# Performance work log

Hardware: AMD Instinct MI355X
Metric: run time of the kernel (lower is better)

The kernel has to match this reference:

```python
import jax, jax.numpy as jnp
import numpy as np

P = 16          # patch_size
EMBED = 768     # embed_dim
HEAD_DIM = 64   # embed_dim // num_heads
ROPE_BASE = 10000.0


def rope_2d(coords, head_dim, base):
    """Axial 2D RoPE. coords: (N, 2) int -> cos, sin each (N, head_dim).
    head_dim is split evenly over the two axes; within an axis, frequency
    pairs are repeated twice (standard rotate-pairs layout)."""
    dpa = head_dim // 2                                   # dims per axis
    inv_freq = 1.0 / (base ** (jnp.arange(0, dpa, 2, dtype=jnp.float32) / dpa))  # (dpa//2,)
    ang = coords.astype(jnp.float32)[:, :, None] * inv_freq[None, None, :]       # (N, 2, dpa//2)
    ang = jnp.repeat(ang, 2, axis=-1).reshape(coords.shape[0], head_dim)          # (N, head_dim)
    return jnp.cos(ang), jnp.sin(ang)


def setup_inputs() -> dict:
    key = jax.random.key(0)
    k1, k2 = jax.random.split(key, 2)
    B, C, H, W = 32, 3, 512, 512
    images = jax.random.normal(k1, (B, C, H, W), dtype=jnp.float32)
    patch_dim = C * P * P
    W_proj = jax.random.normal(k2, (patch_dim, EMBED), dtype=jnp.float32) * (patch_dim ** -0.5)
    b_proj = jnp.zeros((EMBED,), dtype=jnp.float32)
    return {"images": images, "W_proj": W_proj, "b_proj": b_proj}


def reference(images, W_proj, b_proj):
    B, C, H, W = images.shape
    Hp, Wp = H // P, W // P
    N = B * Hp * Wp
    # patchify: c (hp p1) (wp p2) -> (hp wp) (c p1 p2), packed across batch
    x = images.reshape(B, C, Hp, P, Wp, P).transpose(0, 2, 4, 1, 3, 5).reshape(N, C * P * P)
    tokens = x @ W_proj + b_proj                              # (N, EMBED)
    # per-image patch coordinates (identical grid for every image)
    ys, xs = jnp.meshgrid(jnp.arange(Hp), jnp.arange(Wp), indexing='ij')
    coords = jnp.stack([ys, xs], axis=-1).reshape(Hp * Wp, 2)
    patch_coords = jnp.tile(coords, (B, 1))                    # (N, 2)
    rope_cos, rope_sin = rope_2d(patch_coords, HEAD_DIM, ROPE_BASE)
    cu_seqlens = (jnp.arange(B + 1, dtype=jnp.int32) * (Hp * Wp))
    is_patch = jnp.ones((N,), dtype=bool)
    return tokens, cu_seqlens, patch_coords, rope_cos, rope_sin, is_patch
```

## Files before the change

### kernel.cpp

```cpp
#include <hip/hip_runtime.h>
#include <hip/hip_bf16.h>

typedef unsigned short u16;
typedef unsigned int   u32;
typedef __bf16 bf16x8 __attribute__((ext_vector_type(8)));
typedef float  f32x4  __attribute__((ext_vector_type(4)));

#define N_TOK 32768
constexpr long long OFF_TOKENS = 0;
constexpr long long OFF_CU     = 25165824LL;
constexpr long long OFF_COORDS = 25165857LL;
constexpr long long OFF_COS    = 25231393LL;
constexpr long long OFF_SIN    = 27328545LL;
constexpr long long OFF_ISP    = 29425697LL;

__device__ __forceinline__ void split_bf16(float v, u16& h, u16& l) {
    __hip_bfloat16 bh = __float2bfloat16(v);
    float fh = __bfloat162float(bh);
    __hip_bfloat16 bl = __float2bfloat16(v - fh);
    h = __builtin_bit_cast(u16, bh);
    l = __builtin_bit_cast(u16, bl);
}

__device__ __forceinline__ u32 pk2(float lo, float hi) {
    u32 a = (u32)__builtin_bit_cast(u16, __float2bfloat16(lo));
    u32 b = (u32)__builtin_bit_cast(u16, __float2bfloat16(hi));
    return a | (b << 16);
}

__global__ __launch_bounds__(256) void prep_w(const float* __restrict__ W,
                                              u16* __restrict__ wt2) {
    const int bid = blockIdx.x;
    const int bn  = bid / 24;
    const int kt  = bid - bn * 24;
    const int t   = threadIdx.x;
    #pragma unroll
    for (int p = 0; p < 2; p++) {
        const int idx  = t + p * 256;
        const int lane = idx & 63;
        const int j    = (idx >> 6) & 1;
        const int wnq  = idx >> 7;
        const int n    = bn * 128 + wnq * 32 + j * 16 + (lane & 15);
        const int k0   = kt * 32 + (lane >> 4) * 8;
        u16 hv[8], lv[8];
        #pragma unroll
        for (int e = 0; e < 8; e++)
            split_bf16(W[(size_t)(k0 + e) * 768 + n], hv[e], lv[e]);
        uint4 H, L;
        H.x = (u32)hv[0] | ((u32)hv[1] << 16); H.y = (u32)hv[2] | ((u32)hv[3] << 16);
        H.z = (u32)hv[4] | ((u32)hv[5] << 16); H.w = (u32)hv[6] | ((u32)hv[7] << 16);
        L.x = (u32)lv[0] | ((u32)lv[1] << 16); L.y = (u32)lv[2] | ((u32)lv[3] << 16);
        L.z = (u32)lv[4] | ((u32)lv[5] << 16); L.w = (u32)lv[6] | ((u32)lv[7] << 16);
        u16* dst = wt2 + (size_t)bid * 8192 + (((wnq << 12) | (j << 10) | (lane << 4)) >> 1);
        *(uint4*)dst          = H;
        *(uint4*)(dst + 1024) = L;
    }
}

__global__ __launch_bounds__(512, 4) void patch_gemm_mfma(
    const float* __restrict__ img, const u16* __restrict__ wt2,
    const float* __restrict__ bias, float* __restrict__ out)
{
    __shared__ __align__(16) char smem[16384];
    char* pA0 = smem;
    char* pA1 = smem + 8192;

    const int L   = blockIdx.x;
    const int c   = (L & 7) * 192 + (L >> 3);
    const int bm  = c / 6;
    const int bn  = c - bm * 6;
    const int tb  = bn * 24;

    const int tid  = threadIdx.x;
    const int lane = tid & 63;
    const int wid  = tid >> 6;
    const int wm   = (wid >> 2) << 6;
    const int wn   = (wid & 3) << 5;
    const int lr   = lane & 15;
    const int lg   = lane >> 4;

    const int am = tid & 127;
    const int aq = tid >> 7;
    const int m  = bm * 128 + am;
    const int bb = m >> 10;
    const int hp = (m & 1023) >> 5;
    const int wq = m & 31;
    const float* abase = img + (size_t)bb * 786432 + (size_t)hp * 8192 + wq * 16;
    const int a_wb = am * 64 + (((aq >> 1) ^ ((am >> 3) & 1)) << 5) + ((aq & 1) << 4);

    const int a_rd = lr * 64 + (((lg >> 1) ^ ((lr >> 3) & 1)) << 5) + ((lg & 1) << 4);

    const char* bfrag = (const char*)wt2 + ((wid & 3) << 12) + (lane << 4);

    f32x4 acc[4][2];
    #pragma unroll
    for (int i = 0; i < 4; i++)
        #pragma unroll
        for (int j = 0; j < 2; j++) acc[i][j] = {0.f, 0.f, 0.f, 0.f};

    float4 A0a, A0b, A1a, A1b;

#define LOAD_A(ra, rb, T)                                                   \
    {   const float* ap = abase + ((T) >> 3) * 262144 +                     \
            (((T) & 7) * 2 + (aq >> 1)) * 512 + (aq & 1) * 8;               \
        ra = *(const float4*)ap;  rb = *(const float4*)(ap + 4); }

#define CVT_STORE(ra, rb, pdst)                                             \
    {   uint4 Hq;                                                           \
        Hq.x = pk2(ra.x, ra.y); Hq.y = pk2(ra.z, ra.w);                     \
        Hq.z = pk2(rb.x, rb.y); Hq.w = pk2(rb.z, rb.w);                     \
        *(uint4*)((pdst) + a_wb) = Hq; }

#define ITER(T, Ca, Cb, La, Lb, PACV, PAC)                                  \
    {   bf16x8 bhf[2], blf[2];                                              \
        {   const char* s = bfrag + (size_t)(tb + (T)) * 16384;             \
            bhf[0] = *(const bf16x8*)(s);                                   \
            bhf[1] = *(const bf16x8*)(s + 1024);                            \
            blf[0] = *(const bf16x8*)(s + 2048);                            \
            blf[1] = *(const bf16x8*)(s + 3072); }                          \
        if ((T) + 1 < 24) CVT_STORE(Ca, Cb, PACV);                          \
        if ((T) + 2 < 24) LOAD_A(La, Lb, (T) + 2);                          \
        bf16x8 ahf[4];                                                      \
        _Pragma("unroll")                                                   \
        for (int i = 0; i < 4; i++)                                         \
            ahf[i] = *(const bf16x8*)((PAC) + ((wm + i * 16) << 6) + a_rd); \
        _Pragma("unroll")                                                   \
        for (int i = 0; i < 4; i++)                                         \
            _Pragma("unroll")                                               \
            for (int j = 0; j < 2; j++) {                                   \
                acc[i][j] = __builtin_amdgcn_mfma_f32_16x16x32_bf16(ahf[i], bhf[j], acc[i][j], 0, 0, 0); \
                acc[i][j] = __builtin_amdgcn_mfma_f32_16x16x32_bf16(ahf[i], blf[j], acc[i][j], 0, 0, 0); \
            }                                                               \
        asm volatile("s_waitcnt lgkmcnt(0)" ::: "memory");                  \
        __builtin_amdgcn_s_barrier();                                       \
    }

    LOAD_A(A0a, A0b, 0);
    LOAD_A(A1a, A1b, 1);
    CVT_STORE(A0a, A0b, pA0);
    asm volatile("s_waitcnt lgkmcnt(0)" ::: "memory");
    __builtin_amdgcn_s_barrier();

    #pragma unroll 1
    for (int t = 0; t < 24; t += 2) {
        ITER(t,     A1a, A1b, A0a, A0b, pA1, pA0);
        ITER(t + 1, A0a, A0b, A1a, A1b, pA0, pA1);
    }
#undef ITER
#undef LOAD_A
#undef CVT_STORE

    float bv[2];
    #pragma unroll
    for (int j = 0; j < 2; j++) bv[j] = bias[bn * 128 + wn + j * 16 + lr];
    #pragma unroll
    for (int i = 0; i < 4; i++) {
        const int rb = bm * 128 + wm + i * 16 + lg * 4;
        #pragma unroll
        for (int j = 0; j < 2; j++) {
            const int cg = bn * 128 + wn + j * 16 + lr;
            #pragma unroll
            for (int r = 0; r < 4; r++)
                out[OFF_TOKENS + (size_t)(rb + r) * 768 + cg] = acc[i][j][r] + bv[j];
        }
    }
}

__global__ __launch_bounds__(256) void aux_kernel(float* __restrict__ out)
{
    const int idx = blockIdx.x * 256 + threadIdx.x;
    if (idx >= N_TOK * 32) return;
    const int n  = idx >> 5;
    const int jd = idx & 31;

    const int hp = (n & 1023) >> 5;
    const int wp = n & 31;

    const int coord = (jd < 16) ? hp : wp;
    const int j = jd & 15;
    const float freq = exp2f(-(float)j * 0.8304820237218406f);
    float s, c;
    sincosf((float)coord * freq, &s, &c);

    const long long off = (long long)n * 64 + jd * 2;
    *(float2*)(out + OFF_COS + off) = make_float2(c, c);
    *(float2*)(out + OFF_SIN + off) = make_float2(s, s);

    if (jd == 0) {
        out[OFF_COORDS + 2 * (long long)n]     = (float)hp;
        out[OFF_COORDS + 2 * (long long)n + 1] = (float)wp;
        out[OFF_ISP + n] = 1.0f;
    }
    if (jd == 1 && n < 33) {
        out[OFF_CU + n] = (float)(n * 1024);
    }
}

extern "C" void kernel_launch(void* const* d_in, const int* in_sizes, int n_in,
                              void* d_out, int out_size, void* d_ws, size_t ws_size,
                              hipStream_t stream) {
    const float* img  = (const float*)d_in[0];
    const float* W    = (const float*)d_in[1];
    const float* bias = (const float*)d_in[2];
    float* out = (float*)d_out;
    u16* wt2 = (u16*)d_ws;

    prep_w<<<144, 256, 0, stream>>>(W, wt2);

    patch_gemm_mfma<<<1536, 512, 0, stream>>>(img, wt2, bias, out);

    const int aux_elems = N_TOK * 32;
    aux_kernel<<<(aux_elems + 255) / 256, 256, 0, stream>>>(out);
}
```

Before: 275.7 us.

## Prefetch B fragments one tile ahead and change LDS A layout to k-group-major

B-fragment global loads are now double-buffered in registers, issued one k-tile ahead so their latency overlaps the current tile's MFMAs instead of sitting before them. The LDS layout for A is also changed from a row-major, XOR-swizzled layout to one where each 8-element k-group occupies a contiguous 2KB plane indexed by row. This is meant to give conflict-free 16-byte LDS accesses without the swizzle arithmetic. The cost is extra VGPRs for the second B buffer, which could pressure occupancy under the launch bounds of 512 threads and 4 blocks.

Measured after the change: 268.1 us. 1.03x faster.

```diff
diff --git a/kernel.cpp b/kernel.cpp
--- a/kernel.cpp
+++ b/kernel.cpp
@@ -86,9 +86,9 @@
     const int hp = (m & 1023) >> 5;
     const int wq = m & 31;
     const float* abase = img + (size_t)bb * 786432 + (size_t)hp * 8192 + wq * 16;
-    const int a_wb = am * 64 + (((aq >> 1) ^ ((am >> 3) & 1)) << 5) + ((aq & 1) << 4);
-
-    const int a_rd = lr * 64 + (((lg >> 1) ^ ((lr >> 3) & 1)) << 5) + ((lg & 1) << 4);
+    const int a_wb = aq * 2048 + am * 16;
+
+    const int a_rd = lg * 2048 + lr * 16;
 
     const char* bfrag = (const char*)wt2 + ((wid & 3) << 12) + (lane << 4);
 
@@ -99,6 +99,7 @@
         for (int j = 0; j < 2; j++) acc[i][j] = {0.f, 0.f, 0.f, 0.f};
 
     float4 A0a, A0b, A1a, A1b;
+    bf16x8 B0[4], B1[4];
 
 #define LOAD_A(ra, rb, T)                                                   \
     {   const float* ap = abase + ((T) >> 3) * 262144 +                     \
@@ -111,44 +112,52 @@
         Hq.z = pk2(rb.x, rb.y); Hq.w = pk2(rb.z, rb.w);                     \
         *(uint4*)((pdst) + a_wb) = Hq; }
 
-#define ITER(T, Ca, Cb, La, Lb, PACV, PAC)                                  \
-    {   bf16x8 bhf[2], blf[2];                                              \
-        {   const char* s = bfrag + (size_t)(tb + (T)) * 16384;             \
-            bhf[0] = *(const bf16x8*)(s);                                   \
-            bhf[1] = *(const bf16x8*)(s + 1024);                            \
-            blf[0] = *(const bf16x8*)(s + 2048);                            \
-            blf[1] = *(const bf16x8*)(s + 3072); }                          \
-        if ((T) + 1 < 24) CVT_STORE(Ca, Cb, PACV);                          \
-        if ((T) + 2 < 24) LOAD_A(La, Lb, (T) + 2);                          \
-        bf16x8 ahf[4];                                                      \
+#define BLOAD(T, Bv)                                                        \
+    {   const char* s = bfrag + (size_t)(tb + (T)) * 16384;                 \
+        Bv[0] = *(const bf16x8*)(s);                                        \
+        Bv[1] = *(const bf16x8*)(s + 1024);                                 \
+        Bv[2] = *(const bf16x8*)(s + 2048);                                 \
+        Bv[3] = *(const bf16x8*)(s + 3072); }
+
+#define COMPUTE(PAC, Bv)                                                    \
+    {   bf16x8 ahf[4];                                                      \
         _Pragma("unroll")                                                   \
         for (int i = 0; i < 4; i++)                                         \
-            ahf[i] = *(const bf16x8*)((PAC) + ((wm + i * 16) << 6) + a_rd); \
+            ahf[i] = *(const bf16x8*)((PAC) + ((wm + i * 16) << 4) + a_rd); \
         _Pragma("unroll")                                                   \
         for (int i = 0; i < 4; i++)                                         \
             _Pragma("unroll")                                               \
             for (int j = 0; j < 2; j++) {                                   \
-                acc[i][j] = __builtin_amdgcn_mfma_f32_16x16x32_bf16(ahf[i], bhf[j], acc[i][j], 0, 0, 0); \
-                acc[i][j] = __builtin_amdgcn_mfma_f32_16x16x32_bf16(ahf[i], blf[j], acc[i][j], 0, 0, 0); \
-            }                                                               \
+                acc[i][j] = __builtin_amdgcn_mfma_f32_16x16x32_bf16(ahf[i], Bv[j],     acc[i][j], 0, 0, 0); \
+                acc[i][j] = __builtin_amdgcn_mfma_f32_16x16x32_bf16(ahf[i], Bv[j + 2], acc[i][j], 0, 0, 0); \
+            } }
+
+#define ITER(T, Ca, Cb, La, Lb, PACV, PAC, Bnx, Bcur)                       \
+    {   if ((T) + 1 < 24) BLOAD((T) + 1, Bnx);                              \
+        if ((T) + 1 < 24) CVT_STORE(Ca, Cb, PACV);                          \
+        if ((T) + 2 < 24) LOAD_A(La, Lb, (T) + 2);                          \
+        COMPUTE(PAC, Bcur);                                                 \
         asm volatile("s_waitcnt lgkmcnt(0)" ::: "memory");                  \
         __builtin_amdgcn_s_barrier();                                       \
     }
 
     LOAD_A(A0a, A0b, 0);
     LOAD_A(A1a, A1b, 1);
+    BLOAD(0, B0);
     CVT_STORE(A0a, A0b, pA0);
     asm volatile("s_waitcnt lgkmcnt(0)" ::: "memory");
     __builtin_amdgcn_s_barrier();
 
     #pragma unroll 1
     for (int t = 0; t < 24; t += 2) {
-        ITER(t,     A1a, A1b, A0a, A0b, pA1, pA0);
-        ITER(t + 1, A0a, A0b, A1a, A1b, pA0, pA1);
+        ITER(t,     A1a, A1b, A0a, A0b, pA1, pA0, B1, B0);
+        ITER(t + 1, A0a, A0b, A1a, A1b, pA0, pA1, B0, B1);
     }
 #undef ITER
 #undef LOAD_A
 #undef CVT_STORE
+#undef BLOAD
+#undef COMPUTE
 
     float bv[2];
     #pragma unroll
```

## Stage weight fragments through LDS via async global_load_lds double buffering

Applied to the files above, without the earlier changes.

Weight fragments are no longer loaded straight from global memory into registers each iteration. They are now prefetched one k-step ahead into double-buffered LDS using global_load_lds, and vmcnt waits are tuned so the prefetch overlaps compute. The A-tile LDS layout also changes from an XOR-swizzled row layout to a plain column-group layout. The aim is to hide weight-load latency and cut redundant global traffic, at the cost of three times the shared memory (48KB), which may reduce occupancy below the 4 blocks per CU requested by the launch bounds, and the unswizzled A layout may bring LDS bank conflicts.

After: 256.0 us. 1.08x faster.

```diff
diff --git a/kernel.cpp b/kernel.cpp
--- a/kernel.cpp
+++ b/kernel.cpp
@@ -61,9 +61,11 @@
     const float* __restrict__ img, const u16* __restrict__ wt2,
     const float* __restrict__ bias, float* __restrict__ out)
 {
-    __shared__ __align__(16) char smem[16384];
+    __shared__ __align__(16) char smem[49152];
     char* pA0 = smem;
     char* pA1 = smem + 8192;
+    char* pB0 = smem + 16384;
+    char* pB1 = smem + 32768;
 
     const int L   = blockIdx.x;
     const int c   = (L & 7) * 192 + (L >> 3);
@@ -86,11 +88,11 @@
     const int hp = (m & 1023) >> 5;
     const int wq = m & 31;
     const float* abase = img + (size_t)bb * 786432 + (size_t)hp * 8192 + wq * 16;
-    const int a_wb = am * 64 + (((aq >> 1) ^ ((am >> 3) & 1)) << 5) + ((aq & 1) << 4);
-
-    const int a_rd = lr * 64 + (((lg >> 1) ^ ((lr >> 3) & 1)) << 5) + ((lg & 1) << 4);
-
-    const char* bfrag = (const char*)wt2 + ((wid & 3) << 12) + (lane << 4);
+    const int a_wb = aq * 2048 + am * 16;
+
+    const int a_rd = lg * 2048 + lr * 16;
+
+    const int b_rd = ((wid & 3) << 12) + (lane << 4);
 
     f32x4 acc[4][2];
     #pragma unroll
@@ -111,44 +113,63 @@
         Hq.z = pk2(rb.x, rb.y); Hq.w = pk2(rb.z, rb.w);                     \
         *(uint4*)((pdst) + a_wb) = Hq; }
 
-#define ITER(T, Ca, Cb, La, Lb, PACV, PAC)                                  \
-    {   bf16x8 bhf[2], blf[2];                                              \
-        {   const char* s = bfrag + (size_t)(tb + (T)) * 16384;             \
-            bhf[0] = *(const bf16x8*)(s);                                   \
-            bhf[1] = *(const bf16x8*)(s + 1024);                            \
-            blf[0] = *(const bf16x8*)(s + 2048);                            \
-            blf[1] = *(const bf16x8*)(s + 3072); }                          \
-        if ((T) + 1 < 24) CVT_STORE(Ca, Cb, PACV);                          \
-        if ((T) + 2 < 24) LOAD_A(La, Lb, (T) + 2);                          \
-        bf16x8 ahf[4];                                                      \
+#define GLOADB(T, dst)                                                      \
+    {   const char* s = (const char*)wt2 + (size_t)(tb + (T)) * 16384       \
+                        + (wid << 11) + (lane << 4);                        \
+        char* d = (dst) + (wid << 11);                                      \
+        __builtin_amdgcn_global_load_lds(                                   \
+            (const __attribute__((address_space(1))) u32*)s,                \
+            (__attribute__((address_space(3))) u32*)(d + (lane << 4)), 16, 0, 0); \
+        __builtin_amdgcn_global_load_lds(                                   \
+            (const __attribute__((address_space(1))) u32*)(s + 1024),       \
+            (__attribute__((address_space(3))) u32*)(d + 1024 + (lane << 4)), 16, 0, 0); }
+
+#define COMPUTE(PAC, PBC)                                                   \
+    {   bf16x8 ahf[4], bhf[2], blf[2];                                      \
+        _Pragma("unroll")                                                   \
+        for (int j = 0; j < 2; j++) {                                       \
+            bhf[j] = *(const bf16x8*)((PBC) + b_rd + (j << 10));            \
+            blf[j] = *(const bf16x8*)((PBC) + b_rd + (j << 10) + 2048);     \
+        }                                                                   \
         _Pragma("unroll")                                                   \
         for (int i = 0; i < 4; i++)                                         \
-            ahf[i] = *(const bf16x8*)((PAC) + ((wm + i * 16) << 6) + a_rd); \
+            ahf[i] = *(const bf16x8*)((PAC) + ((wm + i * 16) << 4) + a_rd); \
         _Pragma("unroll")                                                   \
         for (int i = 0; i < 4; i++)                                         \
             _Pragma("unroll")                                               \
             for (int j = 0; j < 2; j++) {                                   \
                 acc[i][j] = __builtin_amdgcn_mfma_f32_16x16x32_bf16(ahf[i], bhf[j], acc[i][j], 0, 0, 0); \
                 acc[i][j] = __builtin_amdgcn_mfma_f32_16x16x32_bf16(ahf[i], blf[j], acc[i][j], 0, 0, 0); \
-            }                                                               \
-        asm volatile("s_waitcnt lgkmcnt(0)" ::: "memory");                  \
+            } }
+
+#define ITER(T, WAITSTR, Ca, Cb, La, Lb, PACV, PAC, PBG, PBC)               \
+    {   if ((T) + 1 < 24) GLOADB((T) + 1, PBG);                             \
+        if ((T) + 2 < 24) LOAD_A(La, Lb, (T) + 2);                          \
+        if ((T) + 1 < 24) CVT_STORE(Ca, Cb, PACV);                          \
+        COMPUTE(PAC, PBC);                                                  \
+        asm volatile("s_waitcnt " WAITSTR " lgkmcnt(0)" ::: "memory");      \
         __builtin_amdgcn_s_barrier();                                       \
     }
 
+    GLOADB(0, pB0);
     LOAD_A(A0a, A0b, 0);
     LOAD_A(A1a, A1b, 1);
     CVT_STORE(A0a, A0b, pA0);
-    asm volatile("s_waitcnt lgkmcnt(0)" ::: "memory");
+    asm volatile("s_waitcnt vmcnt(2) lgkmcnt(0)" ::: "memory");
     __builtin_amdgcn_s_barrier();
 
     #pragma unroll 1
-    for (int t = 0; t < 24; t += 2) {
-        ITER(t,     A1a, A1b, A0a, A0b, pA1, pA0);
-        ITER(t + 1, A0a, A0b, A1a, A1b, pA0, pA1);
-    }
+    for (int t = 0; t < 22; t += 2) {
+        ITER(t,     "vmcnt(2)", A1a, A1b, A0a, A0b, pA1, pA0, pB1, pB0);
+        ITER(t + 1, "vmcnt(2)", A0a, A0b, A1a, A1b, pA0, pA1, pB0, pB1);
+    }
+    ITER(22, "vmcnt(0)", A1a, A1b, A0a, A0b, pA1, pA0, pB1, pB0);
+    ITER(23, "vmcnt(0)", A0a, A0b, A1a, A1b, pA0, pA1, pB0, pB1);
 #undef ITER
 #undef LOAD_A
 #undef CVT_STORE
+#undef GLOADB
+#undef COMPUTE
 
     float bv[2];
     #pragma unroll
```
